# Kernel tuning notes

Measured on AMD Instinct MI355X. Metric: run time of the kernel, lower is better.

## Reference

```python
import jax, jax.numpy as jnp
import numpy as np

B, S, DIN = 2, 2048, 1024
H = 16
DK = 1024   # dim_key_query_all
DV = 1024   # dim_value_all
DOUT = 1024
HEAD_SIZE = DK / H  # attention_head_size (float division in source)
LN_EPS = 1e-5


def setup_inputs() -> dict:
    key = jax.random.key(0)
    ks = jax.random.split(key, 12)
    s_in = 1.0 / np.sqrt(DIN)
    s_dv = 1.0 / np.sqrt(DV)
    return {
        "hidden_states": jax.random.normal(ks[0], (B, S, DIN), jnp.float32),
        "Wq": jax.random.uniform(ks[1], (DK, DIN), jnp.float32, -s_in, s_in),
        "Wk": jax.random.uniform(ks[2], (DK, DIN), jnp.float32, -s_in, s_in),
        "Wcb": jax.random.uniform(ks[3], (H, DIN), jnp.float32, -s_in, s_in),
        "Wv": jax.random.uniform(ks[4], (DV, DIN), jnp.float32, -s_in, s_in),
        "bv": jax.random.uniform(ks[5], (DV,), jnp.float32, -s_in, s_in),
        "mixing": 0.2 * jax.random.normal(ks[6], (H, DK), jnp.float32),
        "Wd": jax.random.uniform(ks[7], (DOUT, DV), jnp.float32, -s_dv, s_dv),
        "bd": jax.random.uniform(ks[8], (DOUT,), jnp.float32, -s_dv, s_dv),
        "gamma": jnp.ones((DV,), jnp.float32),
        "beta": jnp.zeros((DV,), jnp.float32),
    }


def reference(hidden_states, Wq, Wk, Wcb, Wv, bv, mixing, Wd, bd, gamma, beta):
    x = hidden_states  # [B, S, DIN]; self-attention: from == to
    q = jnp.einsum('bsd,kd->bsk', x, Wq)  # [B,S,DK]
    k = jnp.einsum('bsd,kd->bsk', x, Wk)  # [B,S,DK]
    # scores[b,h,i,j] = sum_c q[b,i,c]*mixing[h,c]*k[b,j,c]
    scores = jnp.einsum('bic,hc,bjc->bhij', q, mixing, k)
    cb = jnp.einsum('bjd,hd->bhj', x, Wcb)  # content bias [B,H,S]
    scores = scores + cb[:, :, None, :]
    scores = scores / jnp.sqrt(jnp.asarray(HEAD_SIZE, scores.dtype))
    probs = jax.nn.softmax(scores, axis=-1)  # dropout p=0.0 -> identity
    v = jnp.einsum('bsd,vd->bsv', x, Wv) + bv  # [B,S,DV]
    v = v.reshape(B, S, H, DV // H)
    ctx = jnp.einsum('bhij,bjhv->bihv', probs, v).reshape(B, S, DV)
    out = jnp.einsum('bsv,ov->bso', ctx, Wd) + bd
    res = x + out
    mu = jnp.mean(res, axis=-1, keepdims=True)
    var = jnp.var(res, axis=-1, keepdims=True)
    out = (res - mu) * jax.lax.rsqrt(var + LN_EPS) * gamma + beta
    return (out,)
```

## Files before the change

kernel.cpp:

```cpp
#include <hip/hip_runtime.h>
#include <cstddef>
#include <cstdint>

#define B_    2
#define S_    2048
#define DIN_  1024
#define H_    16
#define DK_   1024
#define DV_   1024
#define DH_   64
#define DOUT_ 1024
#define M_    (B_ * S_)

typedef __attribute__((ext_vector_type(8)))  short short8;
typedef __attribute__((ext_vector_type(4)))  float float4v;
typedef __attribute__((ext_vector_type(16))) float float16v;
typedef _Float16 half8v __attribute__((ext_vector_type(8)));

__device__ __forceinline__ float bf16s_to_f(short s) {
  union { unsigned int u; float f; } cv;
  cv.u = ((unsigned int)(unsigned short)s) << 16;
  return cv.f;
}
__device__ __forceinline__ short f_to_bf16s(float f) {
  union { float f; unsigned int u; } cv;
  cv.f = f;
  unsigned int u = cv.u + 0x7FFFu + ((cv.u >> 16) & 1u);
  return (short)(u >> 16);
}
__device__ __forceinline__ short f_to_f16s(float f) {
  union { _Float16 h; short s; } cv;
  cv.h = (_Float16)f;
  return cv.s;
}
__device__ __forceinline__ unsigned pkrtz_u32(float a, float b) {
  union { __fp16 __attribute__((ext_vector_type(2))) h2; unsigned u; } cv;
  cv.h2 = __builtin_amdgcn_cvt_pkrtz(a, b);
  return cv.u;
}
__device__ __forceinline__ void gll16(const void* g, void* l) {
  __builtin_amdgcn_global_load_lds(
      (const __attribute__((address_space(1))) unsigned int*)g,
      (__attribute__((address_space(3))) unsigned int*)l, 16, 0, 0);
}

__global__ __launch_bounds__(256) void cast_kernel(const float* __restrict__ in,
                                                   short* __restrict__ out, int n4) {
  int i = blockIdx.x * 256 + threadIdx.x;
  if (i >= n4) return;
  float4 v = ((const float4*)in)[i];
  union { ushort4 u; short s[4]; } o;
  o.s[0] = f_to_bf16s(v.x); o.s[1] = f_to_bf16s(v.y);
  o.s[2] = f_to_bf16s(v.z); o.s[3] = f_to_bf16s(v.w);
  ((ushort4*)out)[i] = o.u;
}

__global__ __launch_bounds__(256) void cb_kernel(const float* __restrict__ x,
                                                 const float* __restrict__ Wcb,
                                                 float* __restrict__ CBs) {
  __shared__ float xs[DIN_];
  const int row = blockIdx.x;
  const int tid = threadIdx.x;
  #pragma unroll
  for (int it = 0; it < 4; ++it)
    xs[tid + it * 256] = x[(size_t)row * DIN_ + tid + it * 256];
  __syncthreads();
  const int lane = tid & 63, w = tid >> 6;
  const float SC = 0.125f * 1.44269504088896f;
  #pragma unroll
  for (int hh = 0; hh < 4; ++hh) {
    const int hidx = w * 4 + hh;
    float p = 0.f;
    for (int c = lane; c < DIN_; c += 64)
      p += xs[c] * Wcb[(size_t)hidx * DIN_ + c];
    #pragma unroll
    for (int mk = 1; mk < 64; mk <<= 1) p += __shfl_xor(p, mk);
    if (lane == 0) {
      const int bb = row / S_, ss = row % S_;
      CBs[((size_t)bb * H_ + hidx) * S_ + ss] = p * SC;
    }
  }
}

__global__ __launch_bounds__(256, 2) void gemm_nt(
    const short* __restrict__ A, const short* __restrict__ Bw,
    const float* __restrict__ bias, const float* __restrict__ resid,
    short* __restrict__ outb, float* __restrict__ outf, int mode) {
  const int KD = 1024, ND = 1024;
  __shared__ short As[64][136];
  __shared__ short Bs[64][136];
  const int tid  = threadIdx.x;
  const int lane = tid & 63;
  const int w    = tid >> 6;
  const int quad = lane >> 4;
  const int l16  = lane & 15;
  const int m0   = blockIdx.y * 64;
  const int n0   = blockIdx.x * 64;
  const int wm   = (w >> 1) * 32;
  const int wn   = (w & 1) * 32;
  const int srow = tid >> 2;
  const int sseg = (tid & 3) * 32;

  const float4v zero = {0.f, 0.f, 0.f, 0.f};
  float4v acc[2][2];
  acc[0][0] = zero; acc[0][1] = zero; acc[1][0] = zero; acc[1][1] = zero;

  for (int k0 = 0; k0 < KD; k0 += 128) {
    short8 ar[4], br[4];
    #pragma unroll
    for (int c = 0; c < 4; ++c) {
      ar[c] = *(const short8*)(A  + (size_t)(m0 + srow) * KD + k0 + sseg + c * 8);
      br[c] = *(const short8*)(Bw + (size_t)(n0 + srow) * KD + k0 + sseg + c * 8);
    }
    __syncthreads();
    #pragma unroll
    for (int c = 0; c < 4; ++c) {
      *(short8*)&As[srow][sseg + c * 8] = ar[c];
      *(short8*)&Bs[srow][sseg + c * 8] = br[c];
    }
    __syncthreads();
    #pragma unroll
    for (int ks = 0; ks < 4; ++ks) {
      short8 af0 = *(short8*)&As[wm + l16][ks * 32 + quad * 8];
      short8 af1 = *(short8*)&As[wm + 16 + l16][ks * 32 + quad * 8];
      short8 bg0 = *(short8*)&Bs[wn + l16][ks * 32 + quad * 8];
      short8 bg1 = *(short8*)&Bs[wn + 16 + l16][ks * 32 + quad * 8];
      acc[0][0] = __builtin_amdgcn_mfma_f32_16x16x32_bf16(af0, bg0, acc[0][0], 0, 0, 0);
      acc[0][1] = __builtin_amdgcn_mfma_f32_16x16x32_bf16(af0, bg1, acc[0][1], 0, 0, 0);
      acc[1][0] = __builtin_amdgcn_mfma_f32_16x16x32_bf16(af1, bg0, acc[1][0], 0, 0, 0);
      acc[1][1] = __builtin_amdgcn_mfma_f32_16x16x32_bf16(af1, bg1, acc[1][1], 0, 0, 0);
    }
  }

  #pragma unroll
  for (int mt = 0; mt < 2; ++mt)
    #pragma unroll
    for (int nt = 0; nt < 2; ++nt)
      #pragma unroll
      for (int r = 0; r < 4; ++r) {
        int row = m0 + wm + mt * 16 + quad * 4 + r;
        int col = n0 + wn + nt * 16 + l16;
        float v = acc[mt][nt][r];
        if (mode == 1 || mode == 5) v += bias[col];
        if (mode == 2)
          outf[(size_t)row * ND + col] = v + bias[col] + resid[(size_t)row * ND + col];
        else if (mode == 5) {
          int bb = row >> 11, ss = row & 2047;
          outb[((size_t)bb * DV_ + col) * S_ + ss] = f_to_f16s(v);
        } else if (mode == 4)
          outb[(size_t)row * ND + col] = f_to_f16s(v);
        else
          outb[(size_t)row * ND + col] = f_to_bf16s(v);
      }
}

__global__ __launch_bounds__(256, 2) void attn_kernel(
    const short* __restrict__ Qf, const short* __restrict__ Kf,
    const short* __restrict__ Vtf, const float* __restrict__ mixing,
    const float* __restrict__ CBs, short* __restrict__ ctxb) {
  __shared__ __align__(16) short KsF[128 * 128];
  __shared__ __align__(16) short Vt[64][136];
  __shared__ __align__(16) short mix_s[DK_];
  __shared__ float cb_s[128];

  const int tid  = threadIdx.x;
  const int lane = tid & 63;
  const int l32  = lane & 31;
  const int l1   = lane >> 5;
  const int w    = tid >> 6;

  const int F    = blockIdx.x;
  const int xcd  = F & 7, rest = F >> 3;
  const int b    = xcd >> 2;
  const int h    = (xcd & 3) * 4 + (rest & 3);
  const int i0   = (rest >> 2) * 128;

  const float SC = 0.125f * 1.44269504088896f;
  for (int c = tid; c < DK_; c += 256) {
    union { _Float16 h; short s; } cv;
    cv.h = (_Float16)(mixing[(size_t)h * DK_ + c] * SC);
    mix_s[c] = cv.s;
  }

  const int iq = i0 + w * 32 + l32;
  const short* qptr  = Qf + ((size_t)b * S_ + iq) * DK_;
  const short* kbase = Kf + (size_t)b * S_ * DK_;
  const short* vtb   = Vtf + ((size_t)b * DV_ + h * DH_) * S_;
  const float* cbp   = CBs + ((size_t)b * H_ + h) * S_;

  float16v accS[4], accO[2];
  #pragma unroll
  for (int g = 0; g < 2; ++g)
    #pragma unroll
    for (int r = 0; r < 16; ++r) accO[g][r] = 0.f;
  float m_run = -1e30f, l_run = 0.f;

  const int drow_l = lane >> 4;
  const int dp     = lane & 15;

  const int vrow = tid >> 2;
  const int vseg = (tid & 3) * 32;

  for (int j0 = 0; j0 < S_; j0 += 128) {
    short8 vreg[4];
    #pragma unroll
    for (int c = 0; c < 4; ++c)
      vreg[c] = *(const short8*)(vtb + (size_t)vrow * S_ + j0 + vseg + c * 8);
    float cbv = 0.f;
    if (tid < 128) cbv = cbp[j0 + tid];
    __syncthreads();
    #pragma unroll
    for (int c = 0; c < 4; ++c)
      *(short8*)&Vt[vrow][vseg + c * 8] = vreg[c];
    if (tid < 128) cb_s[tid] = cbv;

    #pragma unroll
    for (int f = 0; f < 4; ++f)
      #pragma unroll
      for (int r = 0; r < 16; ++r) accS[f][r] = 0.f;

    for (int kc = 0; kc < 8; ++kc) {
      half8v qraw[8];
      #pragma unroll
      for (int ks = 0; ks < 8; ++ks)
        qraw[ks] = *(const half8v*)(qptr + kc * 128 + ks * 16 + l1 * 8);
      __syncthreads();
      #pragma unroll
      for (int cc = 0; cc < 8; ++cc) {
        const int n = w * 8 + cc;
        const int r = 4 * n + drow_l;
        const int lchunk = dp ^ (r & 15);
        gll16(kbase + (size_t)(j0 + r) * DK_ + kc * 128 + lchunk * 8,
              &KsF[n * 512]);
      }
      __syncthreads();

      #pragma unroll
      for (int ks = 0; ks < 8; ++ks) {
        half8v mf = *(half8v*)&mix_s[kc * 128 + ks * 16 + l1 * 8];
        half8v qm = qraw[ks] * mf;
        const int poff = ((2 * ks + l1) ^ (l32 & 15)) * 8 + l32 * 128;
        #pragma unroll
        for (int f = 0; f < 4; ++f) {
          half8v af = *(half8v*)&KsF[f * 4096 + poff];
          accS[f] = __builtin_amdgcn_mfma_f32_32x32x16_f16(af, qm, accS[f], 0, 0, 0);
        }
      }
    }

    float tmax = -1e30f;
    #pragma unroll
    for (int f = 0; f < 4; ++f)
      #pragma unroll
      for (int q = 0; q < 4; ++q) {
        float4 cbq = *(float4*)&cb_s[f * 32 + q * 8 + l1 * 4];
        #pragma unroll
        for (int c = 0; c < 4; ++c) {
          accS[f][4 * q + c] += ((const float*)&cbq)[c];
          tmax = fmaxf(tmax, accS[f][4 * q + c]);
        }
      }
    tmax = fmaxf(tmax, __shfl_xor(tmax, 32));
    const float mnew = fmaxf(m_run, tmax);
    const float alpha = exp2f(m_run - mnew);
    float tsum = 0.f;
    #pragma unroll
    for (int f = 0; f < 4; ++f)
      #pragma unroll
      for (int r = 0; r < 16; ++r) {
        float pv = exp2f(accS[f][r] - mnew);
        accS[f][r] = pv;
        tsum += pv;
      }
    tsum += __shfl_xor(tsum, 32);
    l_run = l_run * alpha + tsum;
    m_run = mnew;
    #pragma unroll
    for (int g = 0; g < 2; ++g)
      #pragma unroll
      for (int r = 0; r < 16; ++r) accO[g][r] *= alpha;

    #pragma unroll
    for (int cpv = 0; cpv < 8; ++cpv) {
      const int t = cpv & 1, fp = cpv >> 1;
      float xo[4], yo[4], lo[4], hi[4];
      #pragma unroll
      for (int c = 0; c < 4; ++c) {
        xo[c] = __shfl_xor(accS[fp][8 * t + c], 32);
        yo[c] = __shfl_xor(accS[fp][8 * t + 4 + c], 32);
      }
      #pragma unroll
      for (int c = 0; c < 4; ++c) {
        lo[c] = l1 ? yo[c] : accS[fp][8 * t + c];
        hi[c] = l1 ? accS[fp][8 * t + 4 + c] : xo[c];
      }
      union { half8v v; unsigned u[4]; } pb;
      pb.u[0] = pkrtz_u32(lo[0], lo[1]);
      pb.u[1] = pkrtz_u32(lo[2], lo[3]);
      pb.u[2] = pkrtz_u32(hi[0], hi[1]);
      pb.u[3] = pkrtz_u32(hi[2], hi[3]);
      #pragma unroll
      for (int g = 0; g < 2; ++g) {
        half8v vf = *(half8v*)&Vt[g * 32 + l32][cpv * 16 + l1 * 8];
        accO[g] = __builtin_amdgcn_mfma_f32_32x32x16_f16(vf, pb.v, accO[g], 0, 0, 0);
      }
    }
  }

  const float rl = 1.0f / l_run;
  short* cbase = ctxb + ((size_t)b * S_ + iq) * DV_ + h * DH_;
  #pragma unroll
  for (int g = 0; g < 2; ++g)
    #pragma unroll
    for (int q = 0; q < 4; ++q) {
      const int dv = g * 32 + 8 * q + 4 * l1;
      union { ushort4 u4; short s[4]; } ov;
      #pragma unroll
      for (int r = 0; r < 4; ++r)
        ov.s[r] = f_to_bf16s(accO[g][4 * q + r] * rl);
      *(ushort4*)(cbase + dv) = ov.u4;
    }
}

__global__ __launch_bounds__(256) void ln_kernel(float* __restrict__ out,
                                                 const float* __restrict__ gamma,
                                                 const float* __restrict__ beta) {
  __shared__ float red[8];
  const int row = blockIdx.x;
  const int tid = threadIdx.x;
  float* p = out + (size_t)row * DOUT_;
  float4 v = ((const float4*)p)[tid];
  float s = v.x + v.y + v.z + v.w;
  #pragma unroll
  for (int mk = 1; mk < 64; mk <<= 1) s += __shfl_xor(s, mk);
  if ((tid & 63) == 0) red[tid >> 6] = s;
  __syncthreads();
  const float mean = (red[0] + red[1] + red[2] + red[3]) * (1.0f / 1024.0f);
  const float d0 = v.x - mean, d1 = v.y - mean, d2 = v.z - mean, d3 = v.w - mean;
  float sq = d0 * d0 + d1 * d1 + d2 * d2 + d3 * d3;
  #pragma unroll
  for (int mk = 1; mk < 64; mk <<= 1) sq += __shfl_xor(sq, mk);
  if ((tid & 63) == 0) red[4 + (tid >> 6)] = sq;
  __syncthreads();
  const float var = (red[4] + red[5] + red[6] + red[7]) * (1.0f / 1024.0f);
  const float rstd = rsqrtf(var + 1e-5f);
  float4 g = ((const float4*)gamma)[tid];
  float4 bt = ((const float4*)beta)[tid];
  float4 o;
  o.x = d0 * rstd * g.x + bt.x;
  o.y = d1 * rstd * g.y + bt.y;
  o.z = d2 * rstd * g.z + bt.z;
  o.w = d3 * rstd * g.w + bt.w;
  ((float4*)p)[tid] = o;
}

extern "C" void kernel_launch(void* const* d_in, const int* in_sizes, int n_in,
                              void* d_out, int out_size, void* d_ws, size_t ws_size,
                              hipStream_t stream) {
  (void)in_sizes; (void)n_in; (void)out_size; (void)ws_size;
  const float* x      = (const float*)d_in[0];
  const float* Wq     = (const float*)d_in[1];
  const float* Wk     = (const float*)d_in[2];
  const float* Wcb    = (const float*)d_in[3];
  const float* Wv     = (const float*)d_in[4];
  const float* bv     = (const float*)d_in[5];
  const float* mixing = (const float*)d_in[6];
  const float* Wd     = (const float*)d_in[7];
  const float* bd     = (const float*)d_in[8];
  const float* gamma  = (const float*)d_in[9];
  const float* beta   = (const float*)d_in[10];
  float* out = (float*)d_out;

  short* p = (short*)d_ws;
  short* xb   = p; p += (size_t)M_ * DIN_;
  short* Qf   = p; p += (size_t)M_ * DK_;
  short* Kf   = p; p += (size_t)M_ * DK_;
  short* Vtf  = p; p += (size_t)B_ * DV_ * S_;
  short* ctxb = p; p += (size_t)M_ * DV_;
  short* Wqb  = p; p += (size_t)DK_ * DIN_;
  short* Wkb  = p; p += (size_t)DK_ * DIN_;
  short* Wvb  = p; p += (size_t)DV_ * DIN_;
  short* Wdb  = p; p += (size_t)DOUT_ * DV_;
  float* CBs  = (float*)p;

  cast_kernel<<<dim3(M_ * DIN_ / 1024), 256, 0, stream>>>(x, xb, M_ * DIN_ / 4);
  cast_kernel<<<dim3(DK_ * DIN_ / 1024), 256, 0, stream>>>(Wq, Wqb, DK_ * DIN_ / 4);
  cast_kernel<<<dim3(DK_ * DIN_ / 1024), 256, 0, stream>>>(Wk, Wkb, DK_ * DIN_ / 4);
  cast_kernel<<<dim3(DV_ * DIN_ / 1024), 256, 0, stream>>>(Wv, Wvb, DV_ * DIN_ / 4);
  cast_kernel<<<dim3(DOUT_ * DV_ / 1024), 256, 0, stream>>>(Wd, Wdb, DOUT_ * DV_ / 4);
  cb_kernel<<<dim3(M_), 256, 0, stream>>>(x, Wcb, CBs);

  dim3 gg(DOUT_ / 64, M_ / 64);
  gemm_nt<<<gg, 256, 0, stream>>>(xb, Wqb, nullptr, nullptr, Qf, nullptr, 4);
  gemm_nt<<<gg, 256, 0, stream>>>(xb, Wkb, nullptr, nullptr, Kf, nullptr, 4);
  gemm_nt<<<gg, 256, 0, stream>>>(xb, Wvb, bv, nullptr, Vtf, nullptr, 5);

  attn_kernel<<<dim3(512), 256, 0, stream>>>(Qf, Kf, Vtf, mixing, CBs, ctxb);

  gemm_nt<<<gg, 256, 0, stream>>>(ctxb, Wdb, bd, x, nullptr, out, 2);
  ln_kernel<<<dim3(M_), 256, 0, stream>>>(out, gamma, beta);
}
```

Measured before the change: 648.4 us.

## Double-buffer K tiles in attention and fuse Q/K/V projections into one launch

```diff
diff --git a/kernel.cpp b/kernel.cpp
--- a/kernel.cpp
+++ b/kernel.cpp
@@ -82,10 +82,83 @@
   }
 }
 
-__global__ __launch_bounds__(256, 2) void gemm_nt(
+__global__ __launch_bounds__(256, 2) void gemm_qkv(
+    const short* __restrict__ A, const short* __restrict__ Wqb,
+    const short* __restrict__ Wkb, const short* __restrict__ Wvb,
+    const float* __restrict__ bv, short* __restrict__ Qf,
+    short* __restrict__ Kf, short* __restrict__ Vtf) {
+  const int KD = 1024;
+  __shared__ short As[64][136];
+  __shared__ short Bs[64][136];
+  const int tid  = threadIdx.x;
+  const int lane = tid & 63;
+  const int w    = tid >> 6;
+  const int quad = lane >> 4;
+  const int l16  = lane & 15;
+  const int sel  = blockIdx.x >> 4;
+  const int n0   = (blockIdx.x & 15) * 64;
+  const int m0   = blockIdx.y * 64;
+  const short* Bw = sel == 0 ? Wqb : (sel == 1 ? Wkb : Wvb);
+  const int wm   = (w >> 1) * 32;
+  const int wn   = (w & 1) * 32;
+  const int srow = tid >> 2;
+  const int sseg = (tid & 3) * 32;
+
+  const float4v zero = {0.f, 0.f, 0.f, 0.f};
+  float4v acc[2][2];
+  acc[0][0] = zero; acc[0][1] = zero; acc[1][0] = zero; acc[1][1] = zero;
+
+  for (int k0 = 0; k0 < KD; k0 += 128) {
+    short8 ar[4], br[4];
+    #pragma unroll
+    for (int c = 0; c < 4; ++c) {
+      ar[c] = *(const short8*)(A  + (size_t)(m0 + srow) * KD + k0 + sseg + c * 8);
+      br[c] = *(const short8*)(Bw + (size_t)(n0 + srow) * KD + k0 + sseg + c * 8);
+    }
+    __syncthreads();
+    #pragma unroll
+    for (int c = 0; c < 4; ++c) {
+      *(short8*)&As[srow][sseg + c * 8] = ar[c];
+      *(short8*)&Bs[srow][sseg + c * 8] = br[c];
+    }
+    __syncthreads();
+    #pragma unroll
+    for (int ks = 0; ks < 4; ++ks) {
+      short8 af0 = *(short8*)&As[wm + l16][ks * 32 + quad * 8];
+      short8 af1 = *(short8*)&As[wm + 16 + l16][ks * 32 + quad * 8];
+      short8 bg0 = *(short8*)&Bs[wn + l16][ks * 32 + quad * 8];
+      short8 bg1 = *(short8*)&Bs[wn + 16 + l16][ks * 32 + quad * 8];
+      acc[0][0] = __builtin_amdgcn_mfma_f32_16x16x32_bf16(af0, bg0, acc[0][0], 0, 0, 0);
+      acc[0][1] = __builtin_amdgcn_mfma_f32_16x16x32_bf16(af0, bg1, acc[0][1], 0, 0, 0);
+      acc[1][0] = __builtin_amdgcn_mfma_f32_16x16x32_bf16(af1, bg0, acc[1][0], 0, 0, 0);
+      acc[1][1] = __builtin_amdgcn_mfma_f32_16x16x32_bf16(af1, bg1, acc[1][1], 0, 0, 0);
+    }
+  }
+
+  #pragma unroll
+  for (int mt = 0; mt < 2; ++mt)
+    #pragma unroll
+    for (int nt = 0; nt < 2; ++nt)
+      #pragma unroll
+      for (int r = 0; r < 4; ++r) {
+        int row = m0 + wm + mt * 16 + quad * 4 + r;
+        int col = n0 + wn + nt * 16 + l16;
+        float v = acc[mt][nt][r];
+        if (sel == 2) {
+          v += bv[col];
+          int bb = row >> 11, ss = row & 2047;
+          Vtf[((size_t)bb * DV_ + col) * S_ + ss] = f_to_f16s(v);
+        } else {
+          short* o = sel == 0 ? Qf : Kf;
+          o[(size_t)row * 1024 + col] = f_to_f16s(v);
+        }
+      }
+}
+
+__global__ __launch_bounds__(256, 2) void gemm_out(
     const short* __restrict__ A, const short* __restrict__ Bw,
     const float* __restrict__ bias, const float* __restrict__ resid,
-    short* __restrict__ outb, float* __restrict__ outf, int mode) {
+    float* __restrict__ outf) {
   const int KD = 1024, ND = 1024;
   __shared__ short As[64][136];
   __shared__ short Bs[64][136];
@@ -140,17 +213,8 @@
       for (int r = 0; r < 4; ++r) {
         int row = m0 + wm + mt * 16 + quad * 4 + r;
         int col = n0 + wn + nt * 16 + l16;
-        float v = acc[mt][nt][r];
-        if (mode == 1 || mode == 5) v += bias[col];
-        if (mode == 2)
-          outf[(size_t)row * ND + col] = v + bias[col] + resid[(size_t)row * ND + col];
-        else if (mode == 5) {
-          int bb = row >> 11, ss = row & 2047;
-          outb[((size_t)bb * DV_ + col) * S_ + ss] = f_to_f16s(v);
-        } else if (mode == 4)
-          outb[(size_t)row * ND + col] = f_to_f16s(v);
-        else
-          outb[(size_t)row * ND + col] = f_to_bf16s(v);
+        outf[(size_t)row * ND + col] =
+            acc[mt][nt][r] + bias[col] + resid[(size_t)row * ND + col];
       }
 }
 
@@ -158,7 +222,7 @@
     const short* __restrict__ Qf, const short* __restrict__ Kf,
     const short* __restrict__ Vtf, const float* __restrict__ mixing,
     const float* __restrict__ CBs, short* __restrict__ ctxb) {
-  __shared__ __align__(16) short KsF[128 * 128];
+  __shared__ __align__(16) short Kbuf[2][128 * 64];
   __shared__ __align__(16) short Vt[64][136];
   __shared__ __align__(16) short mix_s[DK_];
   __shared__ float cb_s[128];
@@ -195,8 +259,9 @@
     for (int r = 0; r < 16; ++r) accO[g][r] = 0.f;
   float m_run = -1e30f, l_run = 0.f;
 
-  const int drow_l = lane >> 4;
-  const int dp     = lane & 15;
+  const int dr   = lane >> 3;
+  const int lch  = (lane & 7) ^ dr;
+  const int axor = l32 & 7;
 
   const int vrow = tid >> 2;
   const int vseg = (tid & 3) * 32;
@@ -215,36 +280,53 @@
     if (tid < 128) cb_s[tid] = cbv;
 
     #pragma unroll
+    for (int cc = 0; cc < 4; ++cc) {
+      const int n = w * 4 + cc, row = 8 * n + dr;
+      gll16(kbase + (size_t)(j0 + row) * DK_ + lch * 8, &Kbuf[0][n * 512]);
+    }
+    half8v qcur[4];
+    #pragma unroll
+    for (int ks = 0; ks < 4; ++ks)
+      qcur[ks] = *(const half8v*)(qptr + ks * 16 + l1 * 8);
+
+    #pragma unroll
     for (int f = 0; f < 4; ++f)
       #pragma unroll
       for (int r = 0; r < 16; ++r) accS[f][r] = 0.f;
 
-    for (int kc = 0; kc < 8; ++kc) {
-      half8v qraw[8];
-      #pragma unroll
-      for (int ks = 0; ks < 8; ++ks)
-        qraw[ks] = *(const half8v*)(qptr + kc * 128 + ks * 16 + l1 * 8);
+    #pragma unroll 2
+    for (int c = 0; c < 16; ++c) {
       __syncthreads();
-      #pragma unroll
-      for (int cc = 0; cc < 8; ++cc) {
-        const int n = w * 8 + cc;
-        const int r = 4 * n + drow_l;
-        const int lchunk = dp ^ (r & 15);
-        gll16(kbase + (size_t)(j0 + r) * DK_ + kc * 128 + lchunk * 8,
-              &KsF[n * 512]);
-      }
-      __syncthreads();
-
-      #pragma unroll
-      for (int ks = 0; ks < 8; ++ks) {
-        half8v mf = *(half8v*)&mix_s[kc * 128 + ks * 16 + l1 * 8];
-        half8v qm = qraw[ks] * mf;
-        const int poff = ((2 * ks + l1) ^ (l32 & 15)) * 8 + l32 * 128;
+      if (c < 15) {
+        const int cs = c + 1;
+        #pragma unroll
+        for (int cc = 0; cc < 4; ++cc) {
+          const int n = w * 4 + cc, row = 8 * n + dr;
+          gll16(kbase + (size_t)(j0 + row) * DK_ + cs * 64 + lch * 8,
+                &Kbuf[cs & 1][n * 512]);
+        }
+      }
+      half8v qnext[4];
+      if (c < 15) {
+        #pragma unroll
+        for (int ks = 0; ks < 4; ++ks)
+          qnext[ks] = *(const half8v*)(qptr + (c + 1) * 64 + ks * 16 + l1 * 8);
+      }
+      const short* kb = &Kbuf[c & 1][0];
+      #pragma unroll
+      for (int ks = 0; ks < 4; ++ks) {
+        half8v mf = *(half8v*)&mix_s[c * 64 + ks * 16 + l1 * 8];
+        half8v qm = qcur[ks] * mf;
         #pragma unroll
         for (int f = 0; f < 4; ++f) {
-          half8v af = *(half8v*)&KsF[f * 4096 + poff];
+          const int r = f * 32 + l32;
+          half8v af = *(const half8v*)&kb[r * 64 + ((2 * ks + l1) ^ axor) * 8];
           accS[f] = __builtin_amdgcn_mfma_f32_32x32x16_f16(af, qm, accS[f], 0, 0, 0);
         }
+      }
+      if (c < 15) {
+        #pragma unroll
+        for (int ks = 0; ks < 4; ++ks) qcur[ks] = qnext[ks];
       }
     }
 
@@ -390,13 +472,10 @@
   cast_kernel<<<dim3(DOUT_ * DV_ / 1024), 256, 0, stream>>>(Wd, Wdb, DOUT_ * DV_ / 4);
   cb_kernel<<<dim3(M_), 256, 0, stream>>>(x, Wcb, CBs);
 
-  dim3 gg(DOUT_ / 64, M_ / 64);
-  gemm_nt<<<gg, 256, 0, stream>>>(xb, Wqb, nullptr, nullptr, Qf, nullptr, 4);
-  gemm_nt<<<gg, 256, 0, stream>>>(xb, Wkb, nullptr, nullptr, Kf, nullptr, 4);
-  gemm_nt<<<gg, 256, 0, stream>>>(xb, Wvb, bv, nullptr, Vtf, nullptr, 5);
+  gemm_qkv<<<dim3(48, M_ / 64), 256, 0, stream>>>(xb, Wqb, Wkb, Wvb, bv, Qf, Kf, Vtf);
 
   attn_kernel<<<dim3(512), 256, 0, stream>>>(Qf, Kf, Vtf, mixing, CBs, ctxb);
 
-  gemm_nt<<<gg, 256, 0, stream>>>(ctxb, Wdb, bd, x, nullptr, out, 2);
+  gemm_out<<<dim3(16, M_ / 64), 256, 0, stream>>>(ctxb, Wdb, bd, x, out);
   ln_kernel<<<dim3(M_), 256, 0, stream>>>(out, gamma, beta);
 }
```

Result: slower. 661.5 us (+2.0%).
